# Kernel tuning notes

Measured on AMD Instinct MI355X. Metric: run time of the kernel, lower is better.

The kernel has to match this reference:

```python
import jax, jax.numpy as jnp
import numpy as np

N_IN, N_OUT, N_HID, N_RES = 16, 2, 256, 256
B, L = 64, 2048
ALPHA_FAST, ALPHA_SLOW, SIGMA_NEU = 1.0, 0.1, 0.05


def _linear_params(k, n_out, n_in):
    # mimics torch nn.Linear default init: U(-1/sqrt(fan_in), 1/sqrt(fan_in))
    bound = 1.0 / np.sqrt(n_in)
    kw, kb = jax.random.split(k)
    W = jax.random.uniform(kw, (n_out, n_in), minval=-bound, maxval=bound, dtype=jnp.float32)
    b = jax.random.uniform(kb, (n_out,), minval=-bound, maxval=bound, dtype=jnp.float32)
    return W, b


def setup_inputs() -> dict:
    key = jax.random.key(0)
    ks = jax.random.split(key, 11)
    W_in, b_in = _linear_params(ks[0], N_HID, N_IN)
    W_hh, b_hh = _linear_params(ks[1], N_HID, N_HID)
    W_sf, b_sf = _linear_params(ks[2], N_HID, N_RES)
    W_fs, b_fs = _linear_params(ks[3], N_RES, N_HID)
    W_res, b_res = _linear_params(ks[4], N_RES, N_RES)
    W_out, b_out = _linear_params(ks[5], N_OUT, N_HID)
    W_pr, b_pr = _linear_params(ks[6], N_IN, N_RES)
    input_signal = jax.random.normal(ks[7], (B, L, N_IN), dtype=jnp.float32)
    hidden = jax.random.normal(ks[8], (B, N_HID), dtype=jnp.float32)
    reservoir = jax.random.normal(ks[9], (B, N_RES), dtype=jnp.float32)
    # neural noise: randn * sigma_neu * sqrt(alpha_fast), precomputed time-major [L,B,H]
    noise = jax.random.normal(ks[10], (L, B, N_HID), dtype=jnp.float32) * (SIGMA_NEU * np.sqrt(ALPHA_FAST))
    return dict(input_signal=input_signal, hidden=hidden, reservoir=reservoir, noise=noise,
                W_in=W_in, b_in=b_in, W_hh=W_hh, b_hh=b_hh, W_sf=W_sf, b_sf=b_sf,
                W_fs=W_fs, b_fs=b_fs, W_res=W_res, b_res=b_res,
                W_out=W_out, b_out=b_out, W_pr=W_pr, b_pr=b_pr, length=L)


def reference(input_signal, hidden, reservoir, noise,
              W_in, b_in, W_hh, b_hh, W_sf, b_sf, W_fs, b_fs,
              W_res, b_res, W_out, b_out, W_pr, b_pr, length):
    xs = jnp.transpose(input_signal, (1, 0, 2))  # [L, B, n_in], time-major like torch permute
    af = jnp.float32(ALPHA_FAST)
    asl = jnp.float32(ALPHA_SLOW)

    def step(carry, inp):
        h, r = carry
        x_t, nz = inp
        tmp_h = jax.nn.relu(x_t @ W_in.T + b_in + h @ W_hh.T + b_hh + r @ W_sf.T + b_sf)
        tmp_r = jax.nn.relu(h @ W_fs.T + b_fs + r @ W_res.T + b_res)
        h = (1.0 - af) * h + af * tmp_h + nz
        r = (1.0 - asl) * r + asl * tmp_r
        out = jnp.clip(h @ W_out.T + b_out, -2.0, 2.0)
        prior = jax.nn.sigmoid(r @ W_pr.T + b_pr)
        return (h, r), (h, out, prior)

    _, (hs, outs, priors) = jax.lax.scan(step, (hidden, reservoir), (xs, noise))
    # back to batch-major [B, L, .]
    return (jnp.transpose(hs, (1, 0, 2)),
            jnp.transpose(outs, (1, 0, 2)),
            jnp.transpose(priors, (1, 0, 2)))
```

## Files before the change

kernel.cpp:

```cpp
#include <hip/hip_runtime.h>
#include <stdint.h>
#include <stddef.h>

#define LT    2048
#define BATCH 64
#define NH    256
#define HS_ELEMS  (BATCH * LT * NH)
#define OUT_ELEMS (BATCH * LT * 2)

typedef __attribute__((ext_vector_type(8))) __bf16 bf16x8;
typedef __attribute__((ext_vector_type(4))) float  f32x4;
typedef __attribute__((ext_vector_type(2))) unsigned u32x2;
typedef __attribute__((ext_vector_type(8))) unsigned short u16x8;

static __device__ __forceinline__ unsigned pk2(float a, float b) {
  unsigned r;
  asm("v_cvt_pk_bf16_f32 %0, %1, %2" : "=v"(r) : "v"(a), "v"(b));
  return r;
}
static __device__ __forceinline__ bf16x8 pack8v(f32x4 a, f32x4 b) {
  union { unsigned u[4]; bf16x8 v; } r;
  r.u[0] = pk2(a[0], a[1]); r.u[1] = pk2(a[2], a[3]);
  r.u[2] = pk2(b[0], b[1]); r.u[3] = pk2(b[2], b[3]);
  return r.v;
}
static __device__ __forceinline__ bf16x8 pack8(const float* p) {
  return pack8v(*(const f32x4*)p, *(const f32x4*)(p + 4));
}
static __device__ __forceinline__ float bf2f(unsigned short u) {
  unsigned v = ((unsigned)u) << 16;
  return __builtin_bit_cast(float, v);
}

#define BARRIER() do {                                           \
    asm volatile("s_waitcnt lgkmcnt(0)" ::: "memory");           \
    __builtin_amdgcn_s_barrier();                                \
    asm volatile("" ::: "memory");                               \
  } while (0)

#define W_RES_OFF 0
#define A_S_OFF   131072
#define BIASR_OFF 147456
#define LDS_BYTES 148480

__global__ __launch_bounds__(256) void u_precompute_kernel(
    const float* __restrict__ x,
    const float* __restrict__ W_in,
    const float* __restrict__ b_in,
    const float* __restrict__ b_hh,
    const float* __restrict__ b_sf,
    float* __restrict__ u)
{
  __shared__ float xs[64][16];
  const int tid = threadIdx.x;
  const int b  = blockIdx.x >> 5;
  const int tc = (blockIdx.x & 31) << 6;
  float w[16];
#pragma unroll
  for (int i = 0; i < 16; ++i) w[i] = W_in[tid * 16 + i];
  const float bias = b_in[tid] + b_hh[tid] + b_sf[tid];
  for (int r = tid; r < 64 * 16; r += 256)
    xs[r >> 4][r & 15] = x[((size_t)b * LT + tc + (r >> 4)) * 16 + (r & 15)];
  __syncthreads();
  for (int tt = 0; tt < 64; ++tt) {
    float s = bias;
#pragma unroll
    for (int i = 0; i < 16; ++i) s += xs[tt][i] * w[i];
    u[((size_t)b * LT + tc + tt) * NH + tid] = s;
  }
}

template<int PRIOR_MODE>
__global__ __launch_bounds__(512, 1) void rnn_seq_kernel(
    const float* __restrict__ hidden,
    const float* __restrict__ reservoir,
    const float* __restrict__ noise,
    const float* __restrict__ W_hh, const float* __restrict__ W_sf,
    const float* __restrict__ W_fs, const float* __restrict__ W_res,
    const float* __restrict__ b_fs, const float* __restrict__ b_res,
    const float* __restrict__ W_pr, const float* __restrict__ b_pr,
    float* __restrict__ hs,
    float* __restrict__ priors,
    u32x2* __restrict__ rws8)
{
  extern __shared__ char lds[];
  const int tid  = threadIdx.x;
  const int lane = tid & 63;
  const int wv   = tid >> 6;
  const int col  = lane & 15;
  const int kg   = lane >> 4;
  const int b0   = blockIdx.x * 16;

#pragma unroll 4
  for (int j = 0; j < 16; ++j) {
    const int c   = j * 512 + tid;
    const int kk8 = c >> 10, n = (c >> 2) & 255, kgs = c & 3;
    *(bf16x8*)(lds + W_RES_OFF + c * 16) =
        pack8(W_res + (size_t)n * NH + kk8 * 32 + kgs * 8);
  }
  {
    const int kk = tid >> 6, l16 = tid & 63;
    const int kgs = l16 >> 4, m = l16 & 15;
    *(bf16x8*)(lds + A_S_OFF + tid * 16) =
        pack8(hidden + (size_t)(b0 + m) * NH + kk * 32 + kgs * 8);
    *(bf16x8*)(lds + A_S_OFF + (tid + 512) * 16) =
        pack8(reservoir + (size_t)(b0 + m) * NH + kk * 32 + kgs * 8);
  }
  if (tid < 64) {
    f32x4 v = *(const f32x4*)(b_fs + tid * 4);
    f32x4 w = *(const f32x4*)(b_res + tid * 4);
    *(f32x4*)(lds + BIASR_OFF + tid * 16) = v + w;
  }

  bf16x8 wHH[2][8], wSF[2][8], wFS[2][8];
#pragma unroll
  for (int tile = 0; tile < 2; ++tile) {
    const int n = wv * 32 + tile * 16 + col;
#pragma unroll
    for (int kk = 0; kk < 8; ++kk) {
      wHH[tile][kk] = pack8(W_hh + (size_t)n * NH + kk * 32 + kg * 8);
      wSF[tile][kk] = pack8(W_sf + (size_t)n * NH + kk * 32 + kg * 8);
      wFS[tile][kk] = pack8(W_fs + (size_t)n * NH + kk * 32 + kg * 8);
    }
  }
  bf16x8 wPR[PRIOR_MODE ? 8 : 1];
  f32x4 bp4;
  if (PRIOR_MODE) {
#pragma unroll
    for (int kk8 = 0; kk8 < 8; ++kk8)
      wPR[kk8] = pack8(W_pr + (size_t)col * NH + kk8 * 32 + kg * 8);
    bp4 = *(const f32x4*)(b_pr + kg * 4);
  }

  const size_t hsRow = (size_t)(b0 + col) * (LT * NH);
  const size_t nzRow = (size_t)(b0 + col) * NH;
  f32x4 r_old[2], accH[2], accR[2], accP;
#pragma unroll
  for (int tile = 0; tile < 2; ++tile) {
    const int nb = wv * 32 + tile * 16 + kg * 4;
    r_old[tile] = *(const f32x4*)(reservoir + nzRow + nb);
    accH[tile]  = *(const f32x4*)(hs + hsRow + nb);
  }
  if (PRIOR_MODE) accP = bp4;

  BARRIER();

#pragma unroll
  for (int tile = 0; tile < 2; ++tile) {
    const int nb = wv * 32 + tile * 16 + kg * 4;
    accR[tile] = *(const f32x4*)(lds + BIASR_OFF + nb * 4);
  }

#pragma unroll 1
  for (int t = 0; t < LT; ++t) {
    const size_t tp1 = (t + 1 < LT) ? (size_t)(t + 1) : (size_t)(LT - 1);
    f32x4 pfU[2], nzc[2];
#pragma unroll
    for (int tile = 0; tile < 2; ++tile) {
      const int nb = wv * 32 + tile * 16 + kg * 4;
      pfU[tile] = *(const f32x4*)(hs + hsRow + tp1 * NH + nb);
      nzc[tile] = *(const f32x4*)(noise + (size_t)t * (BATCH * NH) + nzRow + nb);
    }

    const char* afp = lds + A_S_OFF + lane * 16;
    const char* bwp = lds + W_RES_OFF + (wv * 32) * 64 + col * 64 + kg * 16;
#pragma unroll
    for (int kk = 0; kk < 16; ++kk) {
      const bf16x8 af = *(const bf16x8*)(afp + kk * 1024);
      if (kk < 8) {
#pragma unroll
        for (int tile = 0; tile < 2; ++tile)
          accH[tile] = __builtin_amdgcn_mfma_f32_16x16x32_bf16(wHH[tile][kk], af, accH[tile], 0, 0, 0);
#pragma unroll
        for (int tile = 0; tile < 2; ++tile)
          accR[tile] = __builtin_amdgcn_mfma_f32_16x16x32_bf16(wFS[tile][kk], af, accR[tile], 0, 0, 0);
      } else {
#pragma unroll
        for (int tile = 0; tile < 2; ++tile)
          accH[tile] = __builtin_amdgcn_mfma_f32_16x16x32_bf16(wSF[tile][kk - 8], af, accH[tile], 0, 0, 0);
#pragma unroll
        for (int tile = 0; tile < 2; ++tile) {
          const bf16x8 bw = *(const bf16x8*)(bwp + (kk - 8) * 16384 + tile * 1024);
          accR[tile] = __builtin_amdgcn_mfma_f32_16x16x32_bf16(bw, af, accR[tile], 0, 0, 0);
        }
        if (PRIOR_MODE && wv == 1) {
          accP = __builtin_amdgcn_mfma_f32_16x16x32_bf16(wPR[kk - 8], af, accP, 0, 0, 0);
        }
      }
    }
    BARRIER();

    float* hsT = hs + hsRow + (size_t)t * NH;
    char* abase = lds + A_S_OFF + wv * 1024 + col * 16 + (kg & 1) * 8;
#pragma unroll
    for (int tile = 0; tile < 2; ++tile) {
      const int nb = wv * 32 + tile * 16 + kg * 4;
      f32x4 hv, rv;
#pragma unroll
      for (int j = 0; j < 4; ++j) {
        hv[j] = fmaxf(accH[tile][j], 0.f) + nzc[tile][j];
        rv[j] = 0.9f * r_old[tile][j] + 0.1f * fmaxf(accR[tile][j], 0.f);
      }
      r_old[tile] = rv;
      *(f32x4*)(hsT + nb) = hv;
      u32x2 hp, rp;
      hp[0] = pk2(hv[0], hv[1]); hp[1] = pk2(hv[2], hv[3]);
      rp[0] = pk2(rv[0], rv[1]); rp[1] = pk2(rv[2], rv[3]);
      char* dst = abase + (2 * tile + (kg >> 1)) * 256;
      *(u32x2*)dst          = hp;
      *(u32x2*)(dst + 8192) = rp;
      if (!PRIOR_MODE)
        rws8[((size_t)blockIdx.x * LT + t) * 1024 + tile * 512 + tid] = rp;
    }
    if (PRIOR_MODE && wv == 1 && t > 0) {
      f32x4 pv;
#pragma unroll
      for (int j = 0; j < 4; ++j) pv[j] = 1.f / (1.f + __expf(-accP[j]));
      *(f32x4*)(priors + (size_t)(b0 + col) * (LT * 16) + (size_t)(t - 1) * 16 + kg * 4) = pv;
    }

#pragma unroll
    for (int tile = 0; tile < 2; ++tile) {
      const int nb = wv * 32 + tile * 16 + kg * 4;
      accH[tile] = pfU[tile];
      accR[tile] = *(const f32x4*)(lds + BIASR_OFF + nb * 4);
    }
    if (PRIOR_MODE) accP = bp4;
    BARRIER();
  }

  if (PRIOR_MODE && wv == 1) {
    f32x4 aP = bp4;
    const char* afp2 = lds + A_S_OFF + 8192 + lane * 16;
#pragma unroll
    for (int kk8 = 0; kk8 < 8; ++kk8) {
      const bf16x8 af = *(const bf16x8*)(afp2 + kk8 * 1024);
      aP = __builtin_amdgcn_mfma_f32_16x16x32_bf16(wPR[kk8], af, aP, 0, 0, 0);
    }
    f32x4 pv;
#pragma unroll
    for (int j = 0; j < 4; ++j) pv[j] = 1.f / (1.f + __expf(-aP[j]));
    *(f32x4*)(priors + (size_t)(b0 + col) * (LT * 16) + (size_t)(LT - 1) * 16 + kg * 4) = pv;
  }
}

__global__ __launch_bounds__(256) void prior_post_kernel(
    const u32x2* __restrict__ rws8,
    const float* __restrict__ W_pr,
    const float* __restrict__ b_pr,
    float* __restrict__ priors)
{
  __shared__ unsigned short rs[8 * 16 * 256];
  const int tid = threadIdx.x;
  const int wg = blockIdx.x >> 8;
  const int t0 = (blockIdx.x & 255) * 8;
#pragma unroll 4
  for (int i = 0; i < 32; ++i) {
    const int ci = i * 256 + tid;
    const int tt = ci >> 10, c = ci & 1023;
    const u32x2 v = rws8[((size_t)wg * LT + t0 + tt) * 1024 + c];
    const int tile = c >> 9, t2 = c & 511;
    const int wvv = t2 >> 6, kgg = (t2 >> 4) & 3, cl = t2 & 15;
    const int n0 = wvv * 32 + tile * 16 + kgg * 4;
    *(u32x2*)(rs + ((tt * 16 + cl) << 8) + n0) = v;
  }
  __syncthreads();
  const int n = tid & 15, g = tid >> 4;
  const float* wrow = W_pr + n * NH;
  const float bp = b_pr[n];
  for (int pp = 0; pp < 8; ++pp) {
    const int p = g * 8 + pp;
    const int tt = p >> 4, cl = p & 15;
    const unsigned short* rr = rs + ((tt * 16 + cl) << 8);
    float s = bp;
#pragma unroll 8
    for (int k8 = 0; k8 < 32; ++k8) {
      const f32x4 w0 = *(const f32x4*)(wrow + k8 * 8);
      const f32x4 w1 = *(const f32x4*)(wrow + k8 * 8 + 4);
      const u16x8 a = *(const u16x8*)(rr + k8 * 8);
#pragma unroll
      for (int j = 0; j < 4; ++j)
        s += bf2f(a[j]) * w0[j] + bf2f(a[j + 4]) * w1[j];
    }
    priors[((size_t)(wg * 16 + cl) * LT + t0 + tt) * 16 + n] =
        1.f / (1.f + __expf(-s));
  }
}

__global__ __launch_bounds__(256) void out_project_kernel(
    const float* __restrict__ hs,
    const float* __restrict__ W_out,
    const float* __restrict__ b_out,
    float* __restrict__ outs)
{
  const int tid = threadIdx.x;
  const int lane = tid & 63;
  const int wv = tid >> 6;
  const int row0 = blockIdx.x * 64 + wv * 16;
  f32x4 w0 = *(const f32x4*)(W_out + lane * 4);
  f32x4 w1 = *(const f32x4*)(W_out + 256 + lane * 4);
  const float bo0 = b_out[0], bo1 = b_out[1];
  for (int i = 0; i < 16; ++i) {
    const f32x4 h = *(const f32x4*)(hs + (size_t)(row0 + i) * NH + lane * 4);
    float p0 = h[0]*w0[0] + h[1]*w0[1] + h[2]*w0[2] + h[3]*w0[3];
    float p1 = h[0]*w1[0] + h[1]*w1[1] + h[2]*w1[2] + h[3]*w1[3];
#pragma unroll
    for (int off = 32; off; off >>= 1) {
      p0 += __shfl_down(p0, off, 64);
      p1 += __shfl_down(p1, off, 64);
    }
    if (lane == 0) {
      const size_t o = (size_t)(row0 + i) * 2;
      outs[o]     = fminf(fmaxf(p0 + bo0, -2.f), 2.f);
      outs[o + 1] = fminf(fmaxf(p1 + bo1, -2.f), 2.f);
    }
  }
}

extern "C" void kernel_launch(void* const* d_in, const int* in_sizes, int n_in,
                              void* d_out, int out_size, void* d_ws, size_t ws_size,
                              hipStream_t stream) {
  const float* x         = (const float*)d_in[0];
  const float* hidden    = (const float*)d_in[1];
  const float* reservoir = (const float*)d_in[2];
  const float* noise     = (const float*)d_in[3];
  const float* W_in      = (const float*)d_in[4];
  const float* b_in      = (const float*)d_in[5];
  const float* W_hh      = (const float*)d_in[6];
  const float* b_hh      = (const float*)d_in[7];
  const float* W_sf      = (const float*)d_in[8];
  const float* b_sf      = (const float*)d_in[9];
  const float* W_fs      = (const float*)d_in[10];
  const float* b_fs      = (const float*)d_in[11];
  const float* W_res     = (const float*)d_in[12];
  const float* b_res     = (const float*)d_in[13];
  const float* W_out     = (const float*)d_in[14];
  const float* b_out     = (const float*)d_in[15];
  const float* W_pr      = (const float*)d_in[16];
  const float* b_pr      = (const float*)d_in[17];

  float* hs     = (float*)d_out;
  float* outs   = hs + HS_ELEMS;
  float* priors = outs + OUT_ELEMS;
  u32x2* rws8   = (u32x2*)d_ws;

  const size_t rws_bytes = (size_t)BATCH * LT * NH * sizeof(unsigned short);

  u_precompute_kernel<<<2048, 256, 0, stream>>>(x, W_in, b_in, b_hh, b_sf, hs);

  if (ws_size >= rws_bytes) {
    hipFuncSetAttribute((const void*)&rnn_seq_kernel<0>,
                        hipFuncAttributeMaxDynamicSharedMemorySize, LDS_BYTES);
    rnn_seq_kernel<0><<<4, 512, LDS_BYTES, stream>>>(
        hidden, reservoir, noise, W_hh, W_sf, W_fs, W_res,
        b_fs, b_res, W_pr, b_pr, hs, priors, rws8);
    prior_post_kernel<<<1024, 256, 0, stream>>>(rws8, W_pr, b_pr, priors);
  } else {
    hipFuncSetAttribute((const void*)&rnn_seq_kernel<1>,
                        hipFuncAttributeMaxDynamicSharedMemorySize, LDS_BYTES);
    rnn_seq_kernel<1><<<4, 512, LDS_BYTES, stream>>>(
        hidden, reservoir, noise, W_hh, W_sf, W_fs, W_res,
        b_fs, b_res, W_pr, b_pr, hs, priors, rws8);
  }

  out_project_kernel<<<2048, 256, 0, stream>>>(hs, W_out, b_out, outs);
}
```

Measured before the change: 5.596 ms.

## Double-buffer recurrent state in LDS to drop one barrier per timestep

The bf16 hidden and reservoir state used as the MFMA operand now lives in two LDS buffers chosen by timestep parity. Each step reads the current buffer and writes the next one, so the barrier between the matmul reads and the state writeback is removed, leaving one barrier per step. The combined reservoir bias is also kept in registers instead of being reloaded from LDS every step. The cost is 16 KB more LDS and a few more VGPRs in an already register-heavy kernel.

```diff
diff --git a/kernel.cpp b/kernel.cpp
--- a/kernel.cpp
+++ b/kernel.cpp
@@ -39,9 +39,9 @@
   } while (0)
 
 #define W_RES_OFF 0
-#define A_S_OFF   131072
-#define BIASR_OFF 147456
-#define LDS_BYTES 148480
+#define A_S0_OFF  131072
+#define A_S1_OFF  147456
+#define LDS_BYTES 163840
 
 __global__ __launch_bounds__(256) void u_precompute_kernel(
     const float* __restrict__ x,
@@ -101,18 +101,14 @@
   {
     const int kk = tid >> 6, l16 = tid & 63;
     const int kgs = l16 >> 4, m = l16 & 15;
-    *(bf16x8*)(lds + A_S_OFF + tid * 16) =
+    *(bf16x8*)(lds + A_S0_OFF + tid * 16) =
         pack8(hidden + (size_t)(b0 + m) * NH + kk * 32 + kgs * 8);
-    *(bf16x8*)(lds + A_S_OFF + (tid + 512) * 16) =
+    *(bf16x8*)(lds + A_S0_OFF + (tid + 512) * 16) =
         pack8(reservoir + (size_t)(b0 + m) * NH + kk * 32 + kgs * 8);
   }
-  if (tid < 64) {
-    f32x4 v = *(const f32x4*)(b_fs + tid * 4);
-    f32x4 w = *(const f32x4*)(b_res + tid * 4);
-    *(f32x4*)(lds + BIASR_OFF + tid * 16) = v + w;
-  }
 
   bf16x8 wHH[2][8], wSF[2][8], wFS[2][8];
+  f32x4 biasrR[2];
 #pragma unroll
   for (int tile = 0; tile < 2; ++tile) {
     const int n = wv * 32 + tile * 16 + col;
@@ -122,6 +118,10 @@
       wSF[tile][kk] = pack8(W_sf + (size_t)n * NH + kk * 32 + kg * 8);
       wFS[tile][kk] = pack8(W_fs + (size_t)n * NH + kk * 32 + kg * 8);
     }
+    const int nb = wv * 32 + tile * 16 + kg * 4;
+    f32x4 bf = *(const f32x4*)(b_fs + nb);
+    f32x4 br = *(const f32x4*)(b_res + nb);
+    biasrR[tile] = bf + br;
   }
   bf16x8 wPR[PRIOR_MODE ? 8 : 1];
   f32x4 bp4;
@@ -140,16 +140,11 @@
     const int nb = wv * 32 + tile * 16 + kg * 4;
     r_old[tile] = *(const f32x4*)(reservoir + nzRow + nb);
     accH[tile]  = *(const f32x4*)(hs + hsRow + nb);
+    accR[tile]  = biasrR[tile];
   }
   if (PRIOR_MODE) accP = bp4;
 
   BARRIER();
-
-#pragma unroll
-  for (int tile = 0; tile < 2; ++tile) {
-    const int nb = wv * 32 + tile * 16 + kg * 4;
-    accR[tile] = *(const f32x4*)(lds + BIASR_OFF + nb * 4);
-  }
 
 #pragma unroll 1
   for (int t = 0; t < LT; ++t) {
@@ -162,7 +157,7 @@
       nzc[tile] = *(const f32x4*)(noise + (size_t)t * (BATCH * NH) + nzRow + nb);
     }
 
-    const char* afp = lds + A_S_OFF + lane * 16;
+    const char* afp = lds + A_S0_OFF + ((t & 1) << 14) + lane * 16;
     const char* bwp = lds + W_RES_OFF + (wv * 32) * 64 + col * 64 + kg * 16;
 #pragma unroll
     for (int kk = 0; kk < 16; ++kk) {
@@ -188,10 +183,10 @@
         }
       }
     }
-    BARRIER();
 
     float* hsT = hs + hsRow + (size_t)t * NH;
-    char* abase = lds + A_S_OFF + wv * 1024 + col * 16 + (kg & 1) * 8;
+    char* abase = lds + A_S0_OFF + (((t + 1) & 1) << 14) +
+                  wv * 1024 + col * 16 + (kg & 1) * 8;
 #pragma unroll
     for (int tile = 0; tile < 2; ++tile) {
       const int nb = wv * 32 + tile * 16 + kg * 4;
@@ -221,9 +216,8 @@
 
 #pragma unroll
     for (int tile = 0; tile < 2; ++tile) {
-      const int nb = wv * 32 + tile * 16 + kg * 4;
       accH[tile] = pfU[tile];
-      accR[tile] = *(const f32x4*)(lds + BIASR_OFF + nb * 4);
+      accR[tile] = biasrR[tile];
     }
     if (PRIOR_MODE) accP = bp4;
     BARRIER();
@@ -231,7 +225,7 @@
 
   if (PRIOR_MODE && wv == 1) {
     f32x4 aP = bp4;
-    const char* afp2 = lds + A_S_OFF + 8192 + lane * 16;
+    const char* afp2 = lds + A_S0_OFF + 8192 + lane * 16;
 #pragma unroll
     for (int kk8 = 0; kk8 < 8; ++kk8) {
       const bf16x8 af = *(const bf16x8*)(afp2 + kk8 * 1024);
```

Result: slower. 6.335 ms (+13.2%).

## Stream half of W_res and W_sf from pre-converted bf16 global buffer each step

Applied to the files above, without the earlier changes.

A new kernel converts W_res and W_sf to bf16 in an MFMA-friendly layout in workspace. The sequential kernel now keeps only half of W_res in LDS and one W_sf tile in registers, and streams the other halves from global or L2 every timestep, interleaved with the MFMAs. The loop is unrolled by two with double-buffered noise and u prefetches issued earlier, and the barrier now uses sched_barrier. This frees registers and LDS on the latency-bound recurrence, at the cost of per-step global loads that can add latency.

```diff
diff --git a/kernel.cpp b/kernel.cpp
--- a/kernel.cpp
+++ b/kernel.cpp
@@ -7,6 +7,8 @@
 #define NH    256
 #define HS_ELEMS  (BATCH * LT * NH)
 #define OUT_ELEMS (BATCH * LT * 2)
+#define WS_DUMP_BYTES   ((size_t)BATCH * LT * NH * 2)
+#define WS_STREAM_BYTES (2 * 131072)
 
 typedef __attribute__((ext_vector_type(8))) __bf16 bf16x8;
 typedef __attribute__((ext_vector_type(4))) float  f32x4;
@@ -35,13 +37,24 @@
 #define BARRIER() do {                                           \
     asm volatile("s_waitcnt lgkmcnt(0)" ::: "memory");           \
     __builtin_amdgcn_s_barrier();                                \
-    asm volatile("" ::: "memory");                               \
+    __builtin_amdgcn_sched_barrier(0);                           \
   } while (0)
 
 #define W_RES_OFF 0
 #define A_S_OFF   131072
 #define BIASR_OFF 147456
 #define LDS_BYTES 148480
+
+__global__ __launch_bounds__(256) void wconvert_kernel(
+    const float* __restrict__ W_res, const float* __restrict__ W_sf,
+    __bf16* __restrict__ dst)
+{
+  const int c = blockIdx.x * 256 + threadIdx.x;
+  const int mat = c >> 13, cc = c & 8191;
+  const int kk8 = cc >> 10, n = (cc >> 2) & 255, kgs = cc & 3;
+  const float* src = (mat ? W_sf : W_res) + (size_t)n * NH + kk8 * 32 + kgs * 8;
+  *(bf16x8*)(dst + (size_t)c * 8) = pack8(src);
+}
 
 __global__ __launch_bounds__(256) void u_precompute_kernel(
     const float* __restrict__ x,
@@ -70,18 +83,16 @@
   }
 }
 
-template<int PRIOR_MODE>
-__global__ __launch_bounds__(512, 1) void rnn_seq_kernel(
+__global__ __launch_bounds__(512, 1) void rnn_seq_stream_kernel(
     const float* __restrict__ hidden,
     const float* __restrict__ reservoir,
     const float* __restrict__ noise,
     const float* __restrict__ W_hh, const float* __restrict__ W_sf,
     const float* __restrict__ W_fs, const float* __restrict__ W_res,
     const float* __restrict__ b_fs, const float* __restrict__ b_res,
-    const float* __restrict__ W_pr, const float* __restrict__ b_pr,
     float* __restrict__ hs,
-    float* __restrict__ priors,
-    u32x2* __restrict__ rws8)
+    u32x2* __restrict__ rws8,
+    const char* __restrict__ wstream)
 {
   extern __shared__ char lds[];
   const int tid  = threadIdx.x;
@@ -95,8 +106,9 @@
   for (int j = 0; j < 16; ++j) {
     const int c   = j * 512 + tid;
     const int kk8 = c >> 10, n = (c >> 2) & 255, kgs = c & 3;
-    *(bf16x8*)(lds + W_RES_OFF + c * 16) =
-        pack8(W_res + (size_t)n * NH + kk8 * 32 + kgs * 8);
+    if ((n & 16) == 0)
+      *(bf16x8*)(lds + W_RES_OFF + c * 16) =
+          pack8(W_res + (size_t)n * NH + kk8 * 32 + kgs * 8);
   }
   {
     const int kk = tid >> 6, l16 = tid & 63;
@@ -112,7 +124,166 @@
     *(f32x4*)(lds + BIASR_OFF + tid * 16) = v + w;
   }
 
-  bf16x8 wHH[2][8], wSF[2][8], wFS[2][8];
+  bf16x8 wHH[2][8], wFS[2][8], wSF0[8];
+#pragma unroll
+  for (int tile = 0; tile < 2; ++tile) {
+    const int n = wv * 32 + tile * 16 + col;
+#pragma unroll
+    for (int kk = 0; kk < 8; ++kk) {
+      wHH[tile][kk] = pack8(W_hh + (size_t)n * NH + kk * 32 + kg * 8);
+      wFS[tile][kk] = pack8(W_fs + (size_t)n * NH + kk * 32 + kg * 8);
+    }
+  }
+  {
+    const int n = wv * 32 + col;
+#pragma unroll
+    for (int kk = 0; kk < 8; ++kk)
+      wSF0[kk] = pack8(W_sf + (size_t)n * NH + kk * 32 + kg * 8);
+  }
+
+  const char* gR = wstream + wv * 2048 + 1024 + col * 64 + kg * 16;
+  const char* gS = gR + 131072;
+
+  const size_t hsRow = (size_t)(b0 + col) * (LT * NH);
+  const size_t nzRow = (size_t)(b0 + col) * NH;
+  f32x4 r_old[2], accH[2], accR[2];
+  f32x4 nzA[2], pfA[2], nzB[2], pfB[2];
+#pragma unroll
+  for (int tile = 0; tile < 2; ++tile) {
+    const int nb = wv * 32 + tile * 16 + kg * 4;
+    r_old[tile] = *(const f32x4*)(reservoir + nzRow + nb);
+    accH[tile]  = *(const f32x4*)(hs + hsRow + nb);
+    nzA[tile]   = *(const f32x4*)(noise + nzRow + nb);
+    pfA[tile]   = *(const f32x4*)(hs + hsRow + NH + nb);
+  }
+
+  BARRIER();
+
+#pragma unroll
+  for (int tile = 0; tile < 2; ++tile) {
+    const int nb = wv * 32 + tile * 16 + kg * 4;
+    accR[tile] = *(const f32x4*)(lds + BIASR_OFF + nb * 4);
+  }
+
+  const char* afp = lds + A_S_OFF + lane * 16;
+  const char* bwp = lds + W_RES_OFF + (wv * 32) * 64 + col * 64 + kg * 16;
+
+#define STEP(T, NZC, PFU, NZN, PFN)                                          \
+  {                                                                          \
+    bf16x8 sR[4], sS[4];                                                     \
+    _Pragma("unroll")                                                        \
+    for (int kk = 0; kk < 16; ++kk) {                                        \
+      if (kk == 12) {    \
+        const size_t tq1 = ((T) + 1 < LT) ? (size_t)((T) + 1) : (LT - 1);    \
+        const size_t tq2 = ((T) + 2 < LT) ? (size_t)((T) + 2) : (LT - 1);    \
+        _Pragma("unroll")                                                    \
+        for (int tile = 0; tile < 2; ++tile) {                               \
+          const int nb = wv * 32 + tile * 16 + kg * 4;                       \
+          NZN[tile] = *(const f32x4*)(noise + tq1 * (BATCH * NH) + nzRow + nb); \
+          PFN[tile] = *(const f32x4*)(hs + hsRow + tq2 * NH + nb);           \
+        }                                                                    \
+      }                                                                      \
+      const bf16x8 af = *(const bf16x8*)(afp + kk * 1024);                   \
+      if (kk >= 4 && kk < 8) {                                               \
+        sR[kk - 4] = *(const bf16x8*)(gR + (kk - 4) * 16384);                \
+        sS[kk - 4] = *(const bf16x8*)(gS + (kk - 4) * 16384);                \
+      }                                                                      \
+      if (kk < 8) {                                                          \
+        accH[0] = __builtin_amdgcn_mfma_f32_16x16x32_bf16(wHH[0][kk], af, accH[0], 0, 0, 0); \
+        accH[1] = __builtin_amdgcn_mfma_f32_16x16x32_bf16(wHH[1][kk], af, accH[1], 0, 0, 0); \
+        accR[0] = __builtin_amdgcn_mfma_f32_16x16x32_bf16(wFS[0][kk], af, accR[0], 0, 0, 0); \
+        accR[1] = __builtin_amdgcn_mfma_f32_16x16x32_bf16(wFS[1][kk], af, accR[1], 0, 0, 0); \
+      } else {                                                               \
+        const int j = kk - 8;                                                \
+        accH[0] = __builtin_amdgcn_mfma_f32_16x16x32_bf16(wSF0[j], af, accH[0], 0, 0, 0); \
+        accH[1] = __builtin_amdgcn_mfma_f32_16x16x32_bf16(sS[j & 3], af, accH[1], 0, 0, 0); \
+        const bf16x8 bw = *(const bf16x8*)(bwp + j * 16384);                 \
+        accR[0] = __builtin_amdgcn_mfma_f32_16x16x32_bf16(bw, af, accR[0], 0, 0, 0); \
+        accR[1] = __builtin_amdgcn_mfma_f32_16x16x32_bf16(sR[j & 3], af, accR[1], 0, 0, 0); \
+        if (kk < 12) {                                                       \
+          sR[j] = *(const bf16x8*)(gR + (j + 4) * 16384);                    \
+          sS[j] = *(const bf16x8*)(gS + (j + 4) * 16384);                    \
+        }                                                                    \
+      }                                                                      \
+    }                                                                        \
+    BARRIER();                   \
+    float* hsT = hs + hsRow + (size_t)(T) * NH;                              \
+    char* abase = lds + A_S_OFF + wv * 1024 + col * 16 + (kg & 1) * 8;       \
+    _Pragma("unroll")                                                        \
+    for (int tile = 0; tile < 2; ++tile) {                                   \
+      const int nb = wv * 32 + tile * 16 + kg * 4;                           \
+      f32x4 hv, rv;                                                          \
+      _Pragma("unroll")                                                      \
+      for (int j = 0; j < 4; ++j) {                                          \
+        hv[j] = fmaxf(accH[tile][j], 0.f) + NZC[tile][j];        \
+        rv[j] = 0.9f * r_old[tile][j] + 0.1f * fmaxf(accR[tile][j], 0.f);    \
+      }                                                                      \
+      r_old[tile] = rv;                                                      \
+      *(f32x4*)(hsT + nb) = hv;                                              \
+      u32x2 hp, rp;                                                          \
+      hp[0] = pk2(hv[0], hv[1]); hp[1] = pk2(hv[2], hv[3]);                  \
+      rp[0] = pk2(rv[0], rv[1]); rp[1] = pk2(rv[2], rv[3]);                  \
+      char* dst = abase + (2 * tile + (kg >> 1)) * 256;                      \
+      *(u32x2*)dst          = hp;                                            \
+      *(u32x2*)(dst + 8192) = rp;                                            \
+      rws8[((size_t)blockIdx.x * LT + (T)) * 1024 + tile * 512 + tid] = rp;  \
+    }                                                                        \
+    _Pragma("unroll")                                                        \
+    for (int tile = 0; tile < 2; ++tile) {                                   \
+      const int nb = wv * 32 + tile * 16 + kg * 4;                           \
+      accH[tile] = PFU[tile];                                    \
+      accR[tile] = *(const f32x4*)(lds + BIASR_OFF + nb * 4);                \
+    }                                                                        \
+    BARRIER();                               \
+  }
+
+#pragma unroll 1
+  for (int t = 0; t < LT; t += 2) {
+    STEP(t,     nzA, pfA, nzB, pfB)
+    STEP(t + 1, nzB, pfB, nzA, pfA)
+  }
+#undef STEP
+}
+
+__global__ __launch_bounds__(512, 1) void rnn_seq_fallback_kernel(
+    const float* __restrict__ hidden, const float* __restrict__ reservoir,
+    const float* __restrict__ noise,
+    const float* __restrict__ W_hh, const float* __restrict__ W_sf,
+    const float* __restrict__ W_fs, const float* __restrict__ W_res,
+    const float* __restrict__ b_fs, const float* __restrict__ b_res,
+    const float* __restrict__ W_pr, const float* __restrict__ b_pr,
+    float* __restrict__ hs, float* __restrict__ priors)
+{
+  extern __shared__ char lds[];
+  const int tid  = threadIdx.x;
+  const int lane = tid & 63;
+  const int wv   = tid >> 6;
+  const int col  = lane & 15;
+  const int kg   = lane >> 4;
+  const int b0   = blockIdx.x * 16;
+
+#pragma unroll 4
+  for (int j = 0; j < 16; ++j) {
+    const int c   = j * 512 + tid;
+    const int kk8 = c >> 10, n = (c >> 2) & 255, kgs = c & 3;
+    *(bf16x8*)(lds + W_RES_OFF + c * 16) =
+        pack8(W_res + (size_t)n * NH + kk8 * 32 + kgs * 8);
+  }
+  {
+    const int kk = tid >> 6, l16 = tid & 63;
+    const int kgs = l16 >> 4, m = l16 & 15;
+    *(bf16x8*)(lds + A_S_OFF + tid * 16) =
+        pack8(hidden + (size_t)(b0 + m) * NH + kk * 32 + kgs * 8);
+    *(bf16x8*)(lds + A_S_OFF + (tid + 512) * 16) =
+        pack8(reservoir + (size_t)(b0 + m) * NH + kk * 32 + kgs * 8);
+  }
+  if (tid < 64) {
+    f32x4 v = *(const f32x4*)(b_fs + tid * 4);
+    f32x4 w = *(const f32x4*)(b_res + tid * 4);
+    *(f32x4*)(lds + BIASR_OFF + tid * 16) = v + w;
+  }
+
+  bf16x8 wHH[2][8], wSF[2][8], wFS[2][8], wPR[8];
 #pragma unroll
   for (int tile = 0; tile < 2; ++tile) {
     const int n = wv * 32 + tile * 16 + col;
@@ -123,14 +294,10 @@
       wFS[tile][kk] = pack8(W_fs + (size_t)n * NH + kk * 32 + kg * 8);
     }
   }
-  bf16x8 wPR[PRIOR_MODE ? 8 : 1];
-  f32x4 bp4;
-  if (PRIOR_MODE) {
-#pragma unroll
-    for (int kk8 = 0; kk8 < 8; ++kk8)
-      wPR[kk8] = pack8(W_pr + (size_t)col * NH + kk8 * 32 + kg * 8);
-    bp4 = *(const f32x4*)(b_pr + kg * 4);
-  }
+#pragma unroll
+  for (int kk8 = 0; kk8 < 8; ++kk8)
+    wPR[kk8] = pack8(W_pr + (size_t)col * NH + kk8 * 32 + kg * 8);
+  const f32x4 bp4 = *(const f32x4*)(b_pr + kg * 4);
 
   const size_t hsRow = (size_t)(b0 + col) * (LT * NH);
   const size_t nzRow = (size_t)(b0 + col) * NH;
@@ -141,10 +308,8 @@
     r_old[tile] = *(const f32x4*)(reservoir + nzRow + nb);
     accH[tile]  = *(const f32x4*)(hs + hsRow + nb);
   }
-  if (PRIOR_MODE) accP = bp4;
-
+  accP = bp4;
   BARRIER();
-
 #pragma unroll
   for (int tile = 0; tile < 2; ++tile) {
     const int nb = wv * 32 + tile * 16 + kg * 4;
@@ -161,7 +326,6 @@
       pfU[tile] = *(const f32x4*)(hs + hsRow + tp1 * NH + nb);
       nzc[tile] = *(const f32x4*)(noise + (size_t)t * (BATCH * NH) + nzRow + nb);
     }
-
     const char* afp = lds + A_S_OFF + lane * 16;
     const char* bwp = lds + W_RES_OFF + (wv * 32) * 64 + col * 64 + kg * 16;
 #pragma unroll
@@ -183,13 +347,11 @@
           const bf16x8 bw = *(const bf16x8*)(bwp + (kk - 8) * 16384 + tile * 1024);
           accR[tile] = __builtin_amdgcn_mfma_f32_16x16x32_bf16(bw, af, accR[tile], 0, 0, 0);
         }
-        if (PRIOR_MODE && wv == 1) {
+        if (wv == 1)
           accP = __builtin_amdgcn_mfma_f32_16x16x32_bf16(wPR[kk - 8], af, accP, 0, 0, 0);
-        }
       }
     }
     BARRIER();
-
     float* hsT = hs + hsRow + (size_t)t * NH;
     char* abase = lds + A_S_OFF + wv * 1024 + col * 16 + (kg & 1) * 8;
 #pragma unroll
@@ -209,27 +371,23 @@
       char* dst = abase + (2 * tile + (kg >> 1)) * 256;
       *(u32x2*)dst          = hp;
       *(u32x2*)(dst + 8192) = rp;
-      if (!PRIOR_MODE)
-        rws8[((size_t)blockIdx.x * LT + t) * 1024 + tile * 512 + tid] = rp;
-    }
-    if (PRIOR_MODE && wv == 1 && t > 0) {
+    }
+    if (wv == 1 && t > 0) {
       f32x4 pv;
 #pragma unroll
       for (int j = 0; j < 4; ++j) pv[j] = 1.f / (1.f + __expf(-accP[j]));
       *(f32x4*)(priors + (size_t)(b0 + col) * (LT * 16) + (size_t)(t - 1) * 16 + kg * 4) = pv;
     }
-
 #pragma unroll
     for (int tile = 0; tile < 2; ++tile) {
       const int nb = wv * 32 + tile * 16 + kg * 4;
       accH[tile] = pfU[tile];
       accR[tile] = *(const f32x4*)(lds + BIASR_OFF + nb * 4);
     }
-    if (PRIOR_MODE) accP = bp4;
+    accP = bp4;
     BARRIER();
   }
-
-  if (PRIOR_MODE && wv == 1) {
+  if (wv == 1) {
     f32x4 aP = bp4;
     const char* afp2 = lds + A_S_OFF + 8192 + lane * 16;
 #pragma unroll
@@ -343,24 +501,24 @@
   float* outs   = hs + HS_ELEMS;
   float* priors = outs + OUT_ELEMS;
   u32x2* rws8   = (u32x2*)d_ws;
-
-  const size_t rws_bytes = (size_t)BATCH * LT * NH * sizeof(unsigned short);
+  char*  wstream = (char*)d_ws + WS_DUMP_BYTES;
 
   u_precompute_kernel<<<2048, 256, 0, stream>>>(x, W_in, b_in, b_hh, b_sf, hs);
 
-  if (ws_size >= rws_bytes) {
-    hipFuncSetAttribute((const void*)&rnn_seq_kernel<0>,
+  if (ws_size >= WS_DUMP_BYTES + WS_STREAM_BYTES) {
+    wconvert_kernel<<<64, 256, 0, stream>>>(W_res, W_sf, (__bf16*)wstream);
+    hipFuncSetAttribute((const void*)rnn_seq_stream_kernel,
                         hipFuncAttributeMaxDynamicSharedMemorySize, LDS_BYTES);
-    rnn_seq_kernel<0><<<4, 512, LDS_BYTES, stream>>>(
+    rnn_seq_stream_kernel<<<4, 512, LDS_BYTES, stream>>>(
         hidden, reservoir, noise, W_hh, W_sf, W_fs, W_res,
-        b_fs, b_res, W_pr, b_pr, hs, priors, rws8);
+        b_fs, b_res, hs, rws8, wstream);
     prior_post_kernel<<<1024, 256, 0, stream>>>(rws8, W_pr, b_pr, priors);
   } else {
-    hipFuncSetAttribute((const void*)&rnn_seq_kernel<1>,
+    hipFuncSetAttribute((const void*)rnn_seq_fallback_kernel,
                         hipFuncAttributeMaxDynamicSharedMemorySize, LDS_BYTES);
-    rnn_seq_kernel<1><<<4, 512, LDS_BYTES, stream>>>(
+    rnn_seq_fallback_kernel<<<4, 512, LDS_BYTES, stream>>>(
         hidden, reservoir, noise, W_hh, W_sf, W_fs, W_res,
-        b_fs, b_res, W_pr, b_pr, hs, priors, rws8);
+        b_fs, b_res, W_pr, b_pr, hs, priors);
   }
 
   out_project_kernel<<<2048, 256, 0, stream>>>(hs, W_out, b_out, outs);
```

New measurement: 12.53 ms. 124% more time.
